# Kernel tuning notes

Measured on AMD Instinct MI355X. Metric: run time of the kernel, lower is better.

Reference implementation:

```python
import jax, jax.numpy as jnp
import numpy as np

B, N = 8, 16384
NPOINT, RADIUS, NSAMPLE, IN_CH = 512, 0.5, 64, 6
EPS = 1e-5


def _sqdist(a, b):
    # a [B,S,3], b [B,N,3] -> [B,S,N] squared euclidean distances
    return (jnp.sum(a * a, -1)[:, :, None] + jnp.sum(b * b, -1)[:, None, :]
            - 2.0 * jnp.einsum('bsd,bnd->bsn', a, b))


def _fps(xyz, npoint):
    # farthest point sampling (deterministic: starts from index 0)
    Bb, Nn, _ = xyz.shape
    def body(carry, _):
        dist, far = carry  # dist [B,N], far [B]
        centroid = jnp.take_along_axis(xyz, far[:, None, None], axis=1)  # [B,1,3]
        d = jnp.sum((xyz - centroid) ** 2, -1)
        dist = jnp.minimum(dist, d)
        return (dist, jnp.argmax(dist, -1).astype(jnp.int32)), far
    init = (jnp.full((Bb, Nn), 1e10, xyz.dtype), jnp.zeros((Bb,), jnp.int32))
    _, idx = jax.lax.scan(body, init, None, length=npoint)
    return idx.T  # [B, npoint]


def _ball_query(radius, nsample, xyz, new_xyz):
    Nn = xyz.shape[1]
    sq = _sqdist(new_xyz, xyz)  # [B,S,N]
    gidx = jnp.where(sq > radius * radius, Nn,
                     jnp.arange(Nn, dtype=jnp.int32)[None, None, :])
    gidx = jnp.sort(gidx, axis=-1)[:, :, :nsample]  # [B,S,K]
    # pad slots (==N) get the first valid index, as in reference torch code
    return jnp.where(gidx == Nn, gidx[:, :, :1], gidx)


def _gather(x, idx):
    # x [B,N,C], idx [B,...] -> [B,...,C]
    return jax.vmap(lambda xb, ib: xb[ib])(x, idx)


def _forward(xyz, points, layers):
    fps_idx = _fps(xyz, NPOINT)
    new_xyz = _gather(xyz, fps_idx)                        # [B,S,3]
    idx = _ball_query(RADIUS, NSAMPLE, xyz, new_xyz)       # [B,S,K]
    grouped_xyz = _gather(xyz, idx) - new_xyz[:, :, None]  # [B,S,K,3]
    grouped_pts = _gather(points, idx)                     # [B,S,K,3]
    h = jnp.concatenate([grouped_xyz, grouped_pts], -1)[..., :IN_CH]  # [B,S,K,6]
    for (W, b, g, beta) in layers:
        # 1x1 Conv2d == per-point linear; BatchNorm2d (train mode) over (B,K,S)
        h = jnp.einsum('bskc,oc->bsko', h, W) + b
        mu = jnp.mean(h, axis=(0, 1, 2))
        var = jnp.var(h, axis=(0, 1, 2))
        h = jax.nn.relu(g * (h - mu) * jax.lax.rsqrt(var + EPS) + beta)
    return new_xyz, jnp.max(h, axis=2)  # [B,S,3], [B,S,C_out]


def setup_inputs() -> dict:
    key = jax.random.key(0)
    ks = jax.random.split(key, 4)
    return {
        'xyz': jax.random.normal(ks[0], (B, N, 3), jnp.float32),
        'points': jax.random.normal(ks[1], (B, N, 3), jnp.float32),
        'W0': jax.random.normal(ks[2], (64, IN_CH), jnp.float32) * (1.0 / np.sqrt(IN_CH)),
        'b0': jnp.zeros((64,), jnp.float32),
        'g0': jnp.ones((64,), jnp.float32),
        'beta0': jnp.zeros((64,), jnp.float32),
        'W1': jax.random.normal(ks[3], (128, 64), jnp.float32) * (1.0 / np.sqrt(64)),
        'b1': jnp.zeros((128,), jnp.float32),
        'g1': jnp.ones((128,), jnp.float32),
        'beta1': jnp.zeros((128,), jnp.float32),
    }


def reference(xyz, points, W0, b0, g0, beta0, W1, b1, g1, beta1):
    layers = [(W0, b0, g0, beta0), (W1, b1, g1, beta1)]
    return _forward(xyz, points, layers)
```

## Files before the change

kernel.cpp:

```cpp
#include <hip/hip_runtime.h>

#define NB    8
#define NPTS  16384
#define NS    512
#define NK    64
#define C1    64
#define C2    128
#define RAD2  0.25f
#define MTOT  (NB*NS*NK)

typedef float v2f __attribute__((ext_vector_type(2)));
typedef __bf16 bfv8 __attribute__((ext_vector_type(8)));
typedef float f32x4 __attribute__((ext_vector_type(4)));

extern __shared__ char dynsmem[];

#define UMAX_DPP(x, CTRL, RM)                                                   \
    do {                                                                        \
        unsigned _m = (unsigned)__builtin_amdgcn_update_dpp((int)(x), (int)(x), \
                                                            CTRL, RM, 0xf, false); \
        x = (x > _m) ? x : _m;                                                  \
    } while (0)
#define UMIN_DPP(x, CTRL, RM)                                                   \
    do {                                                                        \
        unsigned _m = (unsigned)__builtin_amdgcn_update_dpp((int)(x), (int)(x), \
                                                            CTRL, RM, 0xf, false); \
        x = (x < _m) ? x : _m;                                                  \
    } while (0)

__global__ __launch_bounds__(1024, 4) void fps_kernel(const float* __restrict__ xyz,
                                                      float* __restrict__ out) {
#pragma clang fp contract(off)
    int b = blockIdx.x;
    int tid = threadIdx.x;
    int lane = tid & 63;
    int w = tid >> 6;
    const float* base = xyz + (size_t)b * NPTS * 3;
    v2f* yv = (v2f*)dynsmem;
    v2f* zv = yv + 8192;
    __shared__ unsigned svals[2][16];
    __shared__ float4 sred4[2][16];
    v2f pxp[8], ddp[8];
#pragma unroll
    for (int jj = 0; jj < 8; ++jj) {
        int p0 = tid + (jj << 11);
        int p1 = p0 + 1024;
        float x0 = base[p0 * 3 + 0], y0 = base[p0 * 3 + 1], z0 = base[p0 * 3 + 2];
        float x1 = base[p1 * 3 + 0], y1 = base[p1 * 3 + 1], z1 = base[p1 * 3 + 2];
        pxp[jj].x = x0; pxp[jj].y = x1;
        v2f yp; yp.x = y0; yp.y = y1;
        v2f zp; zp.x = z0; zp.y = z1;
        yv[(jj << 10) + tid] = yp;
        zv[(jj << 10) + tid] = zp;
        ddp[jj].x = 1e10f; ddp[jj].y = 1e10f;
    }
    float cx = base[0], cy = base[1], cz = base[2];
    if (tid == 0) {
        float* o = out + (size_t)b * NS * 3;
        o[0] = cx; o[1] = cy; o[2] = cz;
    }
    __syncthreads();
    for (int i = 1; i < NS; ++i) {
        v2f cx2; cx2.x = cx; cx2.y = cx;
        v2f cy2; cy2.x = cy; cy2.y = cy;
        v2f cz2; cz2.x = cz; cz2.y = cz;
        v2f cm0, cm1, cm2, cm3;
        cm0.x = -1.f; cm0.y = -1.f; cm1 = cm0; cm2 = cm0; cm3 = cm0;
#pragma unroll
        for (int jj = 0; jj < 8; ++jj) {
            v2f yp = yv[(jj << 10) + tid];
            v2f zp = zv[(jj << 10) + tid];
            v2f dx = pxp[jj] - cx2;
            v2f dy = yp - cy2;
            v2f dz = zp - cz2;
            v2f d = (dx * dx + dy * dy) + dz * dz;
            v2f nd;
            nd.x = fminf(ddp[jj].x, d.x);
            nd.y = fminf(ddp[jj].y, d.y);
            ddp[jj] = nd;
            if ((jj & 3) == 0) { cm0.x = fmaxf(cm0.x, nd.x); cm0.y = fmaxf(cm0.y, nd.y); }
            if ((jj & 3) == 1) { cm1.x = fmaxf(cm1.x, nd.x); cm1.y = fmaxf(cm1.y, nd.y); }
            if ((jj & 3) == 2) { cm2.x = fmaxf(cm2.x, nd.x); cm2.y = fmaxf(cm2.y, nd.y); }
            if ((jj & 3) == 3) { cm3.x = fmaxf(cm3.x, nd.x); cm3.y = fmaxf(cm3.y, nd.y); }
        }
        v2f m01; m01.x = fmaxf(cm0.x, cm1.x); m01.y = fmaxf(cm0.y, cm1.y);
        v2f m23; m23.x = fmaxf(cm2.x, cm3.x); m23.y = fmaxf(cm2.y, cm3.y);
        float bv = fmaxf(fmaxf(m01.x, m23.x), fmaxf(m01.y, m23.y));
        unsigned vb = (unsigned)__float_as_int(bv);
        UMAX_DPP(vb, 0xB1, 0xf);
        UMAX_DPP(vb, 0x4E, 0xf);
        UMAX_DPP(vb, 0x141, 0xf);
        UMAX_DPP(vb, 0x140, 0xf);
        UMAX_DPP(vb, 0x142, 0xa);
        UMAX_DPP(vb, 0x143, 0xc);
        if (lane == 63) svals[i & 1][w] = vb;
        __syncthreads();
        unsigned wv = svals[i & 1][lane & 15];
        UMAX_DPP(wv, 0xB1, 0xf);
        UMAX_DPP(wv, 0x4E, 0xf);
        UMAX_DPP(wv, 0x141, 0xf);
        UMAX_DPP(wv, 0x140, 0xf);
        float W = __int_as_float((int)wv);
        if (__any(bv == W)) {
            unsigned lidx = 0x7fffffffu;
            float lx = 0.f;
#pragma unroll
            for (int jj = 7; jj >= 0; --jj) {
                if (ddp[jj].y == W) { lidx = (unsigned)(tid + (jj << 11) + 1024); lx = pxp[jj].y; }
                if (ddp[jj].x == W) { lidx = (unsigned)(tid + (jj << 11));        lx = pxp[jj].x; }
            }
            unsigned lm = (lidx == 0x7fffffffu) ? 0u : lidx;
            unsigned slot = ((lm >> 11) << 10) + (lm & 1023u);
            unsigned e4 = ((lm >> 10) & 1u) << 2;
            float ly = *(const float*)((const char*)yv + (size_t)slot * 8 + e4);
            float lz = *(const float*)((const char*)zv + (size_t)slot * 8 + e4);
            unsigned widx = lidx;
            UMIN_DPP(widx, 0xB1, 0xf);
            UMIN_DPP(widx, 0x4E, 0xf);
            UMIN_DPP(widx, 0x141, 0xf);
            UMIN_DPP(widx, 0x140, 0xf);
            UMIN_DPP(widx, 0x142, 0xa);
            UMIN_DPP(widx, 0x143, 0xc);
            unsigned wu = (unsigned)__builtin_amdgcn_readlane((int)widx, 63);
            unsigned long long mk = __ballot(lidx == wu);
            int sl = (int)(__ffsll(mk) - 1);
            float sx = __int_as_float(__builtin_amdgcn_readlane(__float_as_int(lx), sl));
            float sy = __int_as_float(__builtin_amdgcn_readlane(__float_as_int(ly), sl));
            float sz = __int_as_float(__builtin_amdgcn_readlane(__float_as_int(lz), sl));
            if (lane == 0) sred4[i & 1][w] = make_float4(__int_as_float((int)wu), sx, sy, sz);
        } else {
            if (lane == 0) sred4[i & 1][w] = make_float4(__int_as_float(0x7fffffff), 0.f, 0.f, 0.f);
        }
        __syncthreads();
        float4 s4 = sred4[i & 1][lane & 15];
        unsigned ci = (unsigned)__float_as_int(s4.x);
        UMIN_DPP(ci, 0xB1, 0xf);
        UMIN_DPP(ci, 0x4E, 0xf);
        UMIN_DPP(ci, 0x141, 0xf);
        UMIN_DPP(ci, 0x140, 0xf);
        unsigned long long mk2 = __ballot((unsigned)__float_as_int(s4.x) == ci);
        int sl2 = (int)(__ffsll(mk2) - 1);
        cx = __int_as_float(__builtin_amdgcn_readlane(__float_as_int(s4.y), sl2));
        cy = __int_as_float(__builtin_amdgcn_readlane(__float_as_int(s4.z), sl2));
        cz = __int_as_float(__builtin_amdgcn_readlane(__float_as_int(s4.w), sl2));
        if (tid == 0) {
            float* o = out + ((size_t)b * NS + i) * 3;
            o[0] = cx; o[1] = cy; o[2] = cz;
        }
    }
}

__global__ __launch_bounds__(256) void ballq_kernel(const float* __restrict__ xyz,
                                                    const float* __restrict__ pts,
                                                    const float* __restrict__ newxyz,
                                                    float* __restrict__ feat) {
    int w = threadIdx.x >> 6;
    int lane = threadIdx.x & 63;
    int wid = blockIdx.x * 4 + w;
    int b = wid >> 9;
    const float* nx = newxyz + (size_t)wid * 3;
    float cx = nx[0], cy = nx[1], cz = nx[2];
    float sa = __fadd_rn(__fadd_rn(__fmul_rn(cx, cx), __fmul_rn(cy, cy)),
                         __fmul_rn(cz, cz));
    __shared__ int sidx[4][64];
    const float* base = xyz + (size_t)b * NPTS * 3;
    int cnt = 0;
    for (int off = 0; off < NPTS && cnt < NK; off += 64) {
        int p = off + lane;
        float bx = base[p * 3 + 0], by = base[p * 3 + 1], bz = base[p * 3 + 2];
        float sb = __fadd_rn(__fadd_rn(__fmul_rn(bx, bx), __fmul_rn(by, by)),
                             __fmul_rn(bz, bz));
        float dt = __fadd_rn(__fadd_rn(__fmul_rn(cx, bx), __fmul_rn(cy, by)),
                             __fmul_rn(cz, bz));
        float sq = __fsub_rn(__fadd_rn(sa, sb), __fmul_rn(2.0f, dt));
        bool inb = !(sq > RAD2);
        unsigned long long mask = __ballot(inb);
        int pos = cnt + (int)__popcll(mask & ((1ull << lane) - 1ull));
        if (inb && pos < NK) sidx[w][pos] = p;
        cnt += (int)__popcll(mask);
    }
    __syncthreads();
    int filled = cnt < NK ? cnt : NK;
    int sel = (lane < filled) ? lane : 0;
    int p = (filled > 0) ? sidx[w][sel] : 0;
    float gx = base[p * 3 + 0], gy = base[p * 3 + 1], gz = base[p * 3 + 2];
    const float* pb = pts + (size_t)b * NPTS * 3;
    float q0 = pb[p * 3 + 0], q1 = pb[p * 3 + 1], q2 = pb[p * 3 + 2];
    float* fr = feat + ((size_t)wid * NK + lane) * 6;
    fr[0] = __fsub_rn(gx, cx);
    fr[1] = __fsub_rn(gy, cy);
    fr[2] = __fsub_rn(gz, cz);
    fr[3] = q0; fr[4] = q1; fr[5] = q2;
}

__global__ __launch_bounds__(256) void stats0_kernel(const float* __restrict__ feat,
                                                     const float* __restrict__ W0,
                                                     const float* __restrict__ b0,
                                                     float* __restrict__ stats) {
    int lane = threadIdx.x & 63;
    int wid = blockIdx.x * 4 + (threadIdx.x >> 6);
    float w0[6];
#pragma unroll
    for (int j = 0; j < 6; ++j) w0[j] = W0[lane * 6 + j];
    float bb = b0[lane];
    float ssum = 0.f, ssq = 0.f;
    int r0 = wid * 256;
    for (int r = r0; r < r0 + 256; ++r) {
        const float* f = feat + (size_t)r * 6;
        float h = bb;
#pragma unroll
        for (int j = 0; j < 6; ++j) h = fmaf(w0[j], f[j], h);
        ssum += h;
        ssq = fmaf(h, h, ssq);
    }
    atomicAdd(&stats[lane], ssum);
    atomicAdd(&stats[64 + lane], ssq);
}

__global__ void fin0_kernel(const float* __restrict__ g0, const float* __restrict__ be0,
                            float* __restrict__ stats) {
    int c = threadIdx.x;
    const float inv = 1.0f / (float)MTOT;
    float mu = stats[c] * inv;
    float var = fmaxf(stats[64 + c] * inv - mu * mu, 0.f);
    float a = g0[c] * rsqrtf(var + 1e-5f);
    stats[384 + c] = a;
    stats[448 + c] = fmaf(-mu, a, be0[c]);
}

__global__ __launch_bounds__(256) void stats1_kernel(const float* __restrict__ feat,
                                                     const float* __restrict__ W0,
                                                     const float* __restrict__ b0,
                                                     const float* __restrict__ W1,
                                                     const float* __restrict__ b1,
                                                     float* __restrict__ stats) {
    int lane = threadIdx.x & 63;
    int w = threadIdx.x >> 6;
    int half = w & 1;
    int pairG = blockIdx.x * 2 + (w >> 1);
    int ch = half * 64 + lane;
    float w0r[6];
#pragma unroll
    for (int j = 0; j < 6; ++j) w0r[j] = W0[lane * 6 + j];
    float b0v = b0[lane];
    float a0 = stats[384 + lane], c0 = stats[448 + lane];
    float w1r[64];
#pragma unroll
    for (int j = 0; j < 64; ++j) w1r[j] = W1[ch * 64 + j];
    float b1v = b1[ch];
    float ssum = 0.f, ssq = 0.f;
    int r0 = pairG * 128;
    for (int r = r0; r < r0 + 128; ++r) {
        const float* f = feat + (size_t)r * 6;
        float h = b0v;
#pragma unroll
        for (int j = 0; j < 6; ++j) h = fmaf(w0r[j], f[j], h);
        float h0n = fmaxf(fmaf(a0, h, c0), 0.f);
        int hbits = __float_as_int(h0n);
        float a0c = 0.f, a1c = 0.f, a2c = 0.f, a3c = 0.f;
#pragma unroll
        for (int j = 0; j < 64; j += 4) {
            a0c = fmaf(w1r[j + 0], __int_as_float(__builtin_amdgcn_readlane(hbits, j + 0)), a0c);
            a1c = fmaf(w1r[j + 1], __int_as_float(__builtin_amdgcn_readlane(hbits, j + 1)), a1c);
            a2c = fmaf(w1r[j + 2], __int_as_float(__builtin_amdgcn_readlane(hbits, j + 2)), a2c);
            a3c = fmaf(w1r[j + 3], __int_as_float(__builtin_amdgcn_readlane(hbits, j + 3)), a3c);
        }
        float acc = b1v + ((a0c + a1c) + (a2c + a3c));
        ssum += acc;
        ssq = fmaf(acc, acc, ssq);
    }
    atomicAdd(&stats[128 + ch], ssum);
    atomicAdd(&stats[256 + ch], ssq);
}

__global__ void fin1_kernel(const float* __restrict__ g1, const float* __restrict__ be1,
                            float* __restrict__ stats) {
    int c = threadIdx.x;
    const float inv = 1.0f / (float)MTOT;
    float mu = stats[128 + c] * inv;
    float var = fmaxf(stats[256 + c] * inv - mu * mu, 0.f);
    float a = g1[c] * rsqrtf(var + 1e-5f);
    stats[512 + c] = a;
    stats[640 + c] = fmaf(-mu, a, be1[c]);
}

__global__ __launch_bounds__(256) void final_mfma_kernel(const float* __restrict__ feat,
                                                         const float* __restrict__ W0,
                                                         const float* __restrict__ b0,
                                                         const float* __restrict__ W1,
                                                         const float* __restrict__ b1,
                                                         const float* __restrict__ stats,
                                                         float* __restrict__ out) {
    char* lds = dynsmem;
    int tid = threadIdx.x;
    int lane = tid & 63;
    int w = tid >> 6;
    int g = blockIdx.x * 4 + w;
    for (int idx = tid; idx < 8192; idx += 256) {
        int o = idx >> 6, c = idx & 63;
        float v = W1[idx];
        unsigned u = __float_as_uint(v);
        unsigned hi = (u + 0x7fffu + ((u >> 16) & 1u)) >> 16;
        float rem = v - __uint_as_float(hi << 16);
        unsigned ur = __float_as_uint(rem);
        unsigned lo = (ur + 0x7fffu + ((ur >> 16) & 1u)) >> 16;
        int byt = (c * 2) ^ ((o & 7) << 4);
        *(unsigned short*)(lds + o * 128 + byt) = (unsigned short)hi;
        *(unsigned short*)(lds + 16384 + o * 128 + byt) = (unsigned short)lo;
    }
    char* X = lds + 32768 + w * 16384;
    float w0r[6];
#pragma unroll
    for (int j = 0; j < 6; ++j) w0r[j] = W0[lane * 6 + j];
    float b0v = b0[lane];
    float a0 = stats[384 + lane], c0v = stats[448 + lane];
    __syncthreads();
    const float* fb = feat + (size_t)g * 64 * 6;
#pragma unroll 4
    for (int r = 0; r < 64; ++r) {
        const float* f = fb + r * 6;
        float h = b0v;
#pragma unroll
        for (int j = 0; j < 6; ++j) h = fmaf(w0r[j], f[j], h);
        float hn = fmaxf(fmaf(a0, h, c0v), 0.f);
        unsigned u = __float_as_uint(hn);
        unsigned hi = (u + 0x7fffu + ((u >> 16) & 1u)) >> 16;
        float rem = hn - __uint_as_float(hi << 16);
        unsigned ur = __float_as_uint(rem);
        unsigned lo = (ur + 0x7fffu + ((ur >> 16) & 1u)) >> 16;
        int byt = (lane * 2) ^ ((r & 7) << 4);
        *(unsigned short*)(X + r * 128 + byt) = (unsigned short)hi;
        *(unsigned short*)(X + 8192 + r * 128 + byt) = (unsigned short)lo;
    }
    __syncthreads();
    float a1v[8], d1v[8];
#pragma unroll
    for (int tn = 0; tn < 8; ++tn) {
        int o = tn * 16 + (lane & 15);
        float a1 = stats[512 + o];
        a1v[tn] = a1;
        d1v[tn] = fmaf(a1, b1[o], stats[640 + o]);
    }
    float mx[8];
#pragma unroll
    for (int tn = 0; tn < 8; ++tn) mx[tn] = -1e30f;
#pragma unroll
    for (int tm = 0; tm < 4; ++tm) {
        bfv8 Ah[2], Al[2];
#pragma unroll
        for (int tk = 0; tk < 2; ++tk) {
            int r = tm * 16 + (lane & 15);
            int colb = (((lane >> 4) * 16) + tk * 64) ^ ((r & 7) << 4);
            Ah[tk] = *(const bfv8*)(X + r * 128 + colb);
            Al[tk] = *(const bfv8*)(X + 8192 + r * 128 + colb);
        }
#pragma unroll
        for (int tn = 0; tn < 8; ++tn) {
            int o = tn * 16 + (lane & 15);
            f32x4 acc = {0.f, 0.f, 0.f, 0.f};
#pragma unroll
            for (int tk = 0; tk < 2; ++tk) {
                int colb = (((lane >> 4) * 16) + tk * 64) ^ ((o & 7) << 4);
                bfv8 Bh = *(const bfv8*)(lds + o * 128 + colb);
                bfv8 Bl = *(const bfv8*)(lds + 16384 + o * 128 + colb);
                acc = __builtin_amdgcn_mfma_f32_16x16x32_bf16(Ah[tk], Bh, acc, 0, 0, 0);
                acc = __builtin_amdgcn_mfma_f32_16x16x32_bf16(Ah[tk], Bl, acc, 0, 0, 0);
                acc = __builtin_amdgcn_mfma_f32_16x16x32_bf16(Al[tk], Bh, acc, 0, 0, 0);
            }
            float t0 = fmaxf(fmaf(a1v[tn], acc[0], d1v[tn]), 0.f);
            float t1 = fmaxf(fmaf(a1v[tn], acc[1], d1v[tn]), 0.f);
            float t2 = fmaxf(fmaf(a1v[tn], acc[2], d1v[tn]), 0.f);
            float t3 = fmaxf(fmaf(a1v[tn], acc[3], d1v[tn]), 0.f);
            mx[tn] = fmaxf(mx[tn], fmaxf(fmaxf(t0, t1), fmaxf(t2, t3)));
        }
    }
#pragma unroll
    for (int tn = 0; tn < 8; ++tn) {
        float v = mx[tn];
        v = fmaxf(v, __shfl_xor(v, 16));
        v = fmaxf(v, __shfl_xor(v, 32));
        mx[tn] = v;
    }
    if (lane < 16) {
        size_t ob = 12288 + (size_t)g * 128;
#pragma unroll
        for (int tn = 0; tn < 8; ++tn) out[ob + tn * 16 + lane] = mx[tn];
    }
}

extern "C" void kernel_launch(void* const* d_in, const int* in_sizes, int n_in,
                              void* d_out, int out_size, void* d_ws, size_t ws_size,
                              hipStream_t stream) {
    const float* xyz = (const float*)d_in[0];
    const float* pts = (const float*)d_in[1];
    const float* W0  = (const float*)d_in[2];
    const float* b0  = (const float*)d_in[3];
    const float* g0  = (const float*)d_in[4];
    const float* be0 = (const float*)d_in[5];
    const float* W1  = (const float*)d_in[6];
    const float* b1  = (const float*)d_in[7];
    const float* g1  = (const float*)d_in[8];
    const float* be1 = (const float*)d_in[9];
    float* out = (float*)d_out;

    float* feat  = (float*)d_ws;
    float* stats = feat + (size_t)MTOT * 6;

    const int fps_lds = 2 * NPTS * (int)sizeof(float);
    (void)hipFuncSetAttribute(reinterpret_cast<const void*>(fps_kernel),
                              hipFuncAttributeMaxDynamicSharedMemorySize, fps_lds);
    const int fm_lds = 98304;
    (void)hipFuncSetAttribute(reinterpret_cast<const void*>(final_mfma_kernel),
                              hipFuncAttributeMaxDynamicSharedMemorySize, fm_lds);

    (void)hipMemsetAsync(stats, 0, 384 * sizeof(float), stream);
    fps_kernel<<<NB, 1024, fps_lds, stream>>>(xyz, out);
    ballq_kernel<<<1024, 256, 0, stream>>>(xyz, pts, out, feat);
    stats0_kernel<<<256, 256, 0, stream>>>(feat, W0, b0, stats);
    fin0_kernel<<<1, 64, 0, stream>>>(g0, be0, stats);
    stats1_kernel<<<1024, 256, 0, stream>>>(feat, W0, b0, W1, b1, stats);
    fin1_kernel<<<1, 128, 0, stream>>>(g1, be1, stats);
    final_mfma_kernel<<<1024, 256, fm_lds, stream>>>(feat, W0, b0, W1, b1, stats, out);
}
```

Baseline: 1.160 ms.

## Use MFMA for layer-1 stats, fold BN finalize kernels, simplify FPS argmax

```diff
diff --git a/kernel.cpp b/kernel.cpp
--- a/kernel.cpp
+++ b/kernel.cpp
@@ -39,7 +39,7 @@
     v2f* yv = (v2f*)dynsmem;
     v2f* zv = yv + 8192;
     __shared__ unsigned svals[2][16];
-    __shared__ float4 sred4[2][16];
+    __shared__ unsigned sidxs[2][16];
     v2f pxp[8], ddp[8];
 #pragma unroll
     for (int jj = 0; jj < 8; ++jj) {
@@ -101,48 +101,30 @@
         UMAX_DPP(wv, 0x141, 0xf);
         UMAX_DPP(wv, 0x140, 0xf);
         float W = __int_as_float((int)wv);
+        unsigned lidx = 0x7fffffffu;
         if (__any(bv == W)) {
-            unsigned lidx = 0x7fffffffu;
-            float lx = 0.f;
 #pragma unroll
             for (int jj = 7; jj >= 0; --jj) {
-                if (ddp[jj].y == W) { lidx = (unsigned)(tid + (jj << 11) + 1024); lx = pxp[jj].y; }
-                if (ddp[jj].x == W) { lidx = (unsigned)(tid + (jj << 11));        lx = pxp[jj].x; }
+                if (ddp[jj].y == W) lidx = (unsigned)(tid + (jj << 11) + 1024);
+                if (ddp[jj].x == W) lidx = (unsigned)(tid + (jj << 11));
             }
-            unsigned lm = (lidx == 0x7fffffffu) ? 0u : lidx;
-            unsigned slot = ((lm >> 11) << 10) + (lm & 1023u);
-            unsigned e4 = ((lm >> 10) & 1u) << 2;
-            float ly = *(const float*)((const char*)yv + (size_t)slot * 8 + e4);
-            float lz = *(const float*)((const char*)zv + (size_t)slot * 8 + e4);
-            unsigned widx = lidx;
-            UMIN_DPP(widx, 0xB1, 0xf);
-            UMIN_DPP(widx, 0x4E, 0xf);
-            UMIN_DPP(widx, 0x141, 0xf);
-            UMIN_DPP(widx, 0x140, 0xf);
-            UMIN_DPP(widx, 0x142, 0xa);
-            UMIN_DPP(widx, 0x143, 0xc);
-            unsigned wu = (unsigned)__builtin_amdgcn_readlane((int)widx, 63);
-            unsigned long long mk = __ballot(lidx == wu);
-            int sl = (int)(__ffsll(mk) - 1);
-            float sx = __int_as_float(__builtin_amdgcn_readlane(__float_as_int(lx), sl));
-            float sy = __int_as_float(__builtin_amdgcn_readlane(__float_as_int(ly), sl));
-            float sz = __int_as_float(__builtin_amdgcn_readlane(__float_as_int(lz), sl));
-            if (lane == 0) sred4[i & 1][w] = make_float4(__int_as_float((int)wu), sx, sy, sz);
-        } else {
-            if (lane == 0) sred4[i & 1][w] = make_float4(__int_as_float(0x7fffffff), 0.f, 0.f, 0.f);
-        }
+        }
+        UMIN_DPP(lidx, 0xB1, 0xf);
+        UMIN_DPP(lidx, 0x4E, 0xf);
+        UMIN_DPP(lidx, 0x141, 0xf);
+        UMIN_DPP(lidx, 0x140, 0xf);
+        UMIN_DPP(lidx, 0x142, 0xa);
+        UMIN_DPP(lidx, 0x143, 0xc);
+        if (lane == 63) sidxs[i & 1][w] = lidx;
         __syncthreads();
-        float4 s4 = sred4[i & 1][lane & 15];
-        unsigned ci = (unsigned)__float_as_int(s4.x);
+        unsigned ci = sidxs[i & 1][lane & 15];
         UMIN_DPP(ci, 0xB1, 0xf);
         UMIN_DPP(ci, 0x4E, 0xf);
         UMIN_DPP(ci, 0x141, 0xf);
         UMIN_DPP(ci, 0x140, 0xf);
-        unsigned long long mk2 = __ballot((unsigned)__float_as_int(s4.x) == ci);
-        int sl2 = (int)(__ffsll(mk2) - 1);
-        cx = __int_as_float(__builtin_amdgcn_readlane(__float_as_int(s4.y), sl2));
-        cy = __int_as_float(__builtin_amdgcn_readlane(__float_as_int(s4.z), sl2));
-        cz = __int_as_float(__builtin_amdgcn_readlane(__float_as_int(s4.w), sl2));
+        int ii = __builtin_amdgcn_readfirstlane((int)ci);
+        const float* cp = base + (size_t)ii * 3;
+        cx = cp[0]; cy = cp[1]; cz = cp[2];
         if (tid == 0) {
             float* o = out + ((size_t)b * NS + i) * 3;
             o[0] = cx; o[1] = cy; o[2] = cz;
@@ -217,71 +199,126 @@
     atomicAdd(&stats[64 + lane], ssq);
 }
 
-__global__ void fin0_kernel(const float* __restrict__ g0, const float* __restrict__ be0,
-                            float* __restrict__ stats) {
-    int c = threadIdx.x;
+__device__ __forceinline__ void bf16_split(float v, unsigned short& hi, unsigned short& lo) {
+    unsigned u = __float_as_uint(v);
+    unsigned h = (u + 0x7fffu + ((u >> 16) & 1u)) >> 16;
+    float rem = v - __uint_as_float(h << 16);
+    unsigned ur = __float_as_uint(rem);
+    unsigned l = (ur + 0x7fffu + ((ur >> 16) & 1u)) >> 16;
+    hi = (unsigned short)h; lo = (unsigned short)l;
+}
+
+__global__ __launch_bounds__(256) void stats1_mfma_kernel(const float* __restrict__ feat,
+                                                          const float* __restrict__ W0,
+                                                          const float* __restrict__ b0,
+                                                          const float* __restrict__ W1,
+                                                          const float* __restrict__ b1,
+                                                          const float* __restrict__ g0,
+                                                          const float* __restrict__ be0,
+                                                          float* __restrict__ stats) {
+    char* lds = dynsmem;
+    int tid = threadIdx.x;
+    int lane = tid & 63;
+    int w = tid >> 6;
+    int g = blockIdx.x * 4 + w;
+    for (int idx = tid; idx < 8192; idx += 256) {
+        int o = idx >> 6, c = idx & 63;
+        unsigned short hi, lo;
+        bf16_split(W1[idx], hi, lo);
+        int byt = (c * 2) ^ ((o & 7) << 4);
+        *(unsigned short*)(lds + o * 128 + byt) = hi;
+        *(unsigned short*)(lds + 16384 + o * 128 + byt) = lo;
+    }
     const float inv = 1.0f / (float)MTOT;
-    float mu = stats[c] * inv;
-    float var = fmaxf(stats[64 + c] * inv - mu * mu, 0.f);
-    float a = g0[c] * rsqrtf(var + 1e-5f);
-    stats[384 + c] = a;
-    stats[448 + c] = fmaf(-mu, a, be0[c]);
-}
-
-__global__ __launch_bounds__(256) void stats1_kernel(const float* __restrict__ feat,
-                                                     const float* __restrict__ W0,
-                                                     const float* __restrict__ b0,
-                                                     const float* __restrict__ W1,
-                                                     const float* __restrict__ b1,
-                                                     float* __restrict__ stats) {
-    int lane = threadIdx.x & 63;
-    int w = threadIdx.x >> 6;
-    int half = w & 1;
-    int pairG = blockIdx.x * 2 + (w >> 1);
-    int ch = half * 64 + lane;
+    float mu0 = stats[lane] * inv;
+    float var0 = fmaxf(stats[64 + lane] * inv - mu0 * mu0, 0.f);
+    float a0 = g0[lane] * rsqrtf(var0 + 1e-5f);
+    float c0v = fmaf(-mu0, a0, be0[lane]);
     float w0r[6];
 #pragma unroll
     for (int j = 0; j < 6; ++j) w0r[j] = W0[lane * 6 + j];
     float b0v = b0[lane];
-    float a0 = stats[384 + lane], c0 = stats[448 + lane];
-    float w1r[64];
-#pragma unroll
-    for (int j = 0; j < 64; ++j) w1r[j] = W1[ch * 64 + j];
-    float b1v = b1[ch];
-    float ssum = 0.f, ssq = 0.f;
-    int r0 = pairG * 128;
-    for (int r = r0; r < r0 + 128; ++r) {
-        const float* f = feat + (size_t)r * 6;
+    char* X = lds + 32768 + w * 16384;
+    __syncthreads();
+    const float* fb = feat + (size_t)g * 64 * 6;
+#pragma unroll 4
+    for (int r = 0; r < 64; ++r) {
+        const float* f = fb + r * 6;
         float h = b0v;
 #pragma unroll
         for (int j = 0; j < 6; ++j) h = fmaf(w0r[j], f[j], h);
-        float h0n = fmaxf(fmaf(a0, h, c0), 0.f);
-        int hbits = __float_as_int(h0n);
-        float a0c = 0.f, a1c = 0.f, a2c = 0.f, a3c = 0.f;
-#pragma unroll
-        for (int j = 0; j < 64; j += 4) {
-            a0c = fmaf(w1r[j + 0], __int_as_float(__builtin_amdgcn_readlane(hbits, j + 0)), a0c);
-            a1c = fmaf(w1r[j + 1], __int_as_float(__builtin_amdgcn_readlane(hbits, j + 1)), a1c);
-            a2c = fmaf(w1r[j + 2], __int_as_float(__builtin_amdgcn_readlane(hbits, j + 2)), a2c);
-            a3c = fmaf(w1r[j + 3], __int_as_float(__builtin_amdgcn_readlane(hbits, j + 3)), a3c);
-        }
-        float acc = b1v + ((a0c + a1c) + (a2c + a3c));
-        ssum += acc;
-        ssq = fmaf(acc, acc, ssq);
-    }
-    atomicAdd(&stats[128 + ch], ssum);
-    atomicAdd(&stats[256 + ch], ssq);
-}
-
-__global__ void fin1_kernel(const float* __restrict__ g1, const float* __restrict__ be1,
-                            float* __restrict__ stats) {
-    int c = threadIdx.x;
-    const float inv = 1.0f / (float)MTOT;
-    float mu = stats[128 + c] * inv;
-    float var = fmaxf(stats[256 + c] * inv - mu * mu, 0.f);
-    float a = g1[c] * rsqrtf(var + 1e-5f);
-    stats[512 + c] = a;
-    stats[640 + c] = fmaf(-mu, a, be1[c]);
+        float hn = fmaxf(fmaf(a0, h, c0v), 0.f);
+        unsigned short hi, lo;
+        bf16_split(hn, hi, lo);
+        int byt = (lane * 2) ^ ((r & 7) << 4);
+        *(unsigned short*)(X + r * 128 + byt) = hi;
+        *(unsigned short*)(X + 8192 + r * 128 + byt) = lo;
+    }
+    __syncthreads();
+    float b1v[8];
+#pragma unroll
+    for (int tn = 0; tn < 8; ++tn) b1v[tn] = b1[tn * 16 + (lane & 15)];
+    float ssum[8], ssq[8];
+#pragma unroll
+    for (int tn = 0; tn < 8; ++tn) { ssum[tn] = 0.f; ssq[tn] = 0.f; }
+#pragma unroll
+    for (int tm = 0; tm < 4; ++tm) {
+        bfv8 Ah[2], Al[2];
+#pragma unroll
+        for (int tk = 0; tk < 2; ++tk) {
+            int r = tm * 16 + (lane & 15);
+            int colb = (((lane >> 4) * 16) + tk * 64) ^ ((r & 7) << 4);
+            Ah[tk] = *(const bfv8*)(X + r * 128 + colb);
+            Al[tk] = *(const bfv8*)(X + 8192 + r * 128 + colb);
+        }
+#pragma unroll
+        for (int tn = 0; tn < 8; ++tn) {
+            int o = tn * 16 + (lane & 15);
+            f32x4 acc = {0.f, 0.f, 0.f, 0.f};
+#pragma unroll
+            for (int tk = 0; tk < 2; ++tk) {
+                int colb = (((lane >> 4) * 16) + tk * 64) ^ ((o & 7) << 4);
+                bfv8 Bh = *(const bfv8*)(lds + o * 128 + colb);
+                bfv8 Bl = *(const bfv8*)(lds + 16384 + o * 128 + colb);
+                acc = __builtin_amdgcn_mfma_f32_16x16x32_bf16(Ah[tk], Bh, acc, 0, 0, 0);
+                acc = __builtin_amdgcn_mfma_f32_16x16x32_bf16(Ah[tk], Bl, acc, 0, 0, 0);
+                acc = __builtin_amdgcn_mfma_f32_16x16x32_bf16(Al[tk], Bh, acc, 0, 0, 0);
+            }
+#pragma unroll
+            for (int j = 0; j < 4; ++j) {
+                float h1 = acc[j] + b1v[tn];
+                ssum[tn] += h1;
+                ssq[tn] = fmaf(h1, h1, ssq[tn]);
+            }
+        }
+    }
+#pragma unroll
+    for (int tn = 0; tn < 8; ++tn) {
+        ssum[tn] += __shfl_xor(ssum[tn], 16);
+        ssum[tn] += __shfl_xor(ssum[tn], 32);
+        ssq[tn] += __shfl_xor(ssq[tn], 16);
+        ssq[tn] += __shfl_xor(ssq[tn], 32);
+    }
+    __syncthreads();
+    float* psum = (float*)(lds + 32768);
+    float* psq  = (float*)(lds + 32768 + 4096);
+    if (lane < 16) {
+#pragma unroll
+        for (int tn = 0; tn < 8; ++tn) {
+            psum[w * 256 + tn * 16 + lane] = ssum[tn];
+            psq[w * 256 + tn * 16 + lane] = ssq[tn];
+        }
+    }
+    __syncthreads();
+    {
+        int ch = tid;
+        if (ch < 128) {
+            float s = psum[ch] + psum[256 + ch] + psum[512 + ch] + psum[768 + ch];
+            float q = psq[ch] + psq[256 + ch] + psq[512 + ch] + psq[768 + ch];
+            atomicAdd(&stats[128 + ch], s);
+            atomicAdd(&stats[256 + ch], q);
+        }
+    }
 }
 
 __global__ __launch_bounds__(256) void final_mfma_kernel(const float* __restrict__ feat,
@@ -289,6 +326,10 @@
                                                          const float* __restrict__ b0,
                                                          const float* __restrict__ W1,
                                                          const float* __restrict__ b1,
+                                                         const float* __restrict__ g0,
+                                                         const float* __restrict__ be0,
+                                                         const float* __restrict__ g1,
+                                                         const float* __restrict__ be1,
                                                          const float* __restrict__ stats,
                                                          float* __restrict__ out) {
     char* lds = dynsmem;
@@ -298,22 +339,22 @@
     int g = blockIdx.x * 4 + w;
     for (int idx = tid; idx < 8192; idx += 256) {
         int o = idx >> 6, c = idx & 63;
-        float v = W1[idx];
-        unsigned u = __float_as_uint(v);
-        unsigned hi = (u + 0x7fffu + ((u >> 16) & 1u)) >> 16;
-        float rem = v - __uint_as_float(hi << 16);
-        unsigned ur = __float_as_uint(rem);
-        unsigned lo = (ur + 0x7fffu + ((ur >> 16) & 1u)) >> 16;
+        unsigned short hi, lo;
+        bf16_split(W1[idx], hi, lo);
         int byt = (c * 2) ^ ((o & 7) << 4);
-        *(unsigned short*)(lds + o * 128 + byt) = (unsigned short)hi;
-        *(unsigned short*)(lds + 16384 + o * 128 + byt) = (unsigned short)lo;
-    }
-    char* X = lds + 32768 + w * 16384;
+        *(unsigned short*)(lds + o * 128 + byt) = hi;
+        *(unsigned short*)(lds + 16384 + o * 128 + byt) = lo;
+    }
+    const float inv = 1.0f / (float)MTOT;
+    float mu0 = stats[lane] * inv;
+    float var0 = fmaxf(stats[64 + lane] * inv - mu0 * mu0, 0.f);
+    float a0 = g0[lane] * rsqrtf(var0 + 1e-5f);
+    float c0v = fmaf(-mu0, a0, be0[lane]);
     float w0r[6];
 #pragma unroll
     for (int j = 0; j < 6; ++j) w0r[j] = W0[lane * 6 + j];
     float b0v = b0[lane];
-    float a0 = stats[384 + lane], c0v = stats[448 + lane];
+    char* X = lds + 32768 + w * 16384;
     __syncthreads();
     const float* fb = feat + (size_t)g * 64 * 6;
 #pragma unroll 4
@@ -323,23 +364,23 @@
 #pragma unroll
         for (int j = 0; j < 6; ++j) h = fmaf(w0r[j], f[j], h);
         float hn = fmaxf(fmaf(a0, h, c0v), 0.f);
-        unsigned u = __float_as_uint(hn);
-        unsigned hi = (u + 0x7fffu + ((u >> 16) & 1u)) >> 16;
-        float rem = hn - __uint_as_float(hi << 16);
-        unsigned ur = __float_as_uint(rem);
-        unsigned lo = (ur + 0x7fffu + ((ur >> 16) & 1u)) >> 16;
+        unsigned short hi, lo;
+        bf16_split(hn, hi, lo);
         int byt = (lane * 2) ^ ((r & 7) << 4);
-        *(unsigned short*)(X + r * 128 + byt) = (unsigned short)hi;
-        *(unsigned short*)(X + 8192 + r * 128 + byt) = (unsigned short)lo;
+        *(unsigned short*)(X + r * 128 + byt) = hi;
+        *(unsigned short*)(X + 8192 + r * 128 + byt) = lo;
     }
     __syncthreads();
     float a1v[8], d1v[8];
 #pragma unroll
     for (int tn = 0; tn < 8; ++tn) {
         int o = tn * 16 + (lane & 15);
-        float a1 = stats[512 + o];
+        float mu1 = stats[128 + o] * inv;
+        float var1 = fmaxf(stats[256 + o] * inv - mu1 * mu1, 0.f);
+        float a1 = g1[o] * rsqrtf(var1 + 1e-5f);
+        float c1 = fmaf(-mu1, a1, be1[o]);
         a1v[tn] = a1;
-        d1v[tn] = fmaf(a1, b1[o], stats[640 + o]);
+        d1v[tn] = fmaf(a1, b1[o], c1);
     }
     float mx[8];
 #pragma unroll
@@ -410,6 +451,8 @@
     (void)hipFuncSetAttribute(reinterpret_cast<const void*>(fps_kernel),
                               hipFuncAttributeMaxDynamicSharedMemorySize, fps_lds);
     const int fm_lds = 98304;
+    (void)hipFuncSetAttribute(reinterpret_cast<const void*>(stats1_mfma_kernel),
+                              hipFuncAttributeMaxDynamicSharedMemorySize, fm_lds);
     (void)hipFuncSetAttribute(reinterpret_cast<const void*>(final_mfma_kernel),
                               hipFuncAttributeMaxDynamicSharedMemorySize, fm_lds);
 
@@ -417,8 +460,6 @@
     fps_kernel<<<NB, 1024, fps_lds, stream>>>(xyz, out);
     ballq_kernel<<<1024, 256, 0, stream>>>(xyz, pts, out, feat);
     stats0_kernel<<<256, 256, 0, stream>>>(feat, W0, b0, stats);
-    fin0_kernel<<<1, 64, 0, stream>>>(g0, be0, stats);
-    stats1_kernel<<<1024, 256, 0, stream>>>(feat, W0, b0, W1, b1, stats);
-    fin1_kernel<<<1, 128, 0, stream>>>(g1, be1, stats);
-    final_mfma_kernel<<<1024, 256, fm_lds, stream>>>(feat, W0, b0, W1, b1, stats, out);
-}
+    stats1_mfma_kernel<<<1024, 256, fm_lds, stream>>>(feat, W0, b0, W1, b1, g0, be0, stats);
+    final_mfma_kernel<<<1024, 256, fm_lds, stream>>>(feat, W0, b0, W1, b1, g0, be0, g1, be1, stats, out);
+}
```

After: 1.064 ms. 1.09x faster.
